# Optimization experiments

Measured on AMD Instinct MI355X. Metric: run time of the kernel, lower is better.

The kernel has to match this reference:

```python
import jax, jax.numpy as jnp
import numpy as np

H, W = 512, 512
N = H * W
NCLS = 4
D_BI, D_SP = 5, 2
THETA_ALPHA, THETA_BETA, THETA_GAMMA = 80.0, 0.0625, 3.0
BI_COMPAT, SP_COMPAT, COMPATIBILITY = 10.0, 3.0, -1.0
NUM_ITER = 10


def _build_lattice(feats):
    """Permutohedral lattice precompute (numpy, integer index construction).
    feats: [N, d]. Returns os [N,d+1] int32 (1-based), ws [N,d+1] float32,
    bn [d+1, M, 2] int32 (0 = missing neighbor), M."""
    feats = np.asarray(feats, np.float64)
    n, d = feats.shape
    inv_std = np.sqrt(2.0 / 3.0) * (d + 1)
    scale = inv_std / np.sqrt((np.arange(d) + 1.0) * (np.arange(d) + 2.0))
    cf = feats * scale
    # embedding matrix E: elevated = cf @ E.T lies on the hyperplane sum=0
    E = np.zeros((d + 1, d))
    E[0, :] = 1.0
    for j in range(1, d + 1):
        E[j, j:] = 1.0
        E[j, j - 1] = -j
    elevated = cf @ E.T  # [n, d+1]
    greedy = (np.rint(elevated / (d + 1)) * (d + 1)).astype(np.int64)
    diff = elevated - greedy
    idx = np.arange(d + 1)
    upper = idx[None, :] > idx[:, None]
    lower = idx[None, :] < idx[:, None]
    di = diff[:, :, None]
    dj = diff[:, None, :]
    rank = (((dj > di) & upper) | ((dj >= di) & lower)).sum(-1)
    rank = rank + greedy.sum(1, keepdims=True) // (d + 1)
    low = rank < 0
    rank = rank + np.where(low, d + 1, 0)
    greedy = greedy + np.where(low, d + 1, 0)
    high = rank > d
    rank = rank - np.where(high, d + 1, 0)
    greedy = greedy - np.where(high, d + 1, 0)
    # barycentric weights
    bary = np.zeros((n, d + 2))
    v = (elevated - greedy) / (d + 1)
    rows = np.repeat(np.arange(n), d + 1)
    np.add.at(bary, (rows, (d - rank).ravel()), v.ravel())
    np.add.at(bary, (rows, (d + 1 - rank).ravel()), -v.ravel())
    bary[:, 0] += 1.0 + bary[:, d + 1]
    ws = bary[:, : d + 1].astype(np.float32)
    # simplex vertex keys (first d coords; last is implied by zero-sum)
    keys = np.empty((n, d + 1, d), np.int64)
    for r in range(d + 1):
        keys[:, r, :] = (greedy + r - (d + 1) * (rank > d - r))[:, :d]
    flat = keys.reshape(-1, d)
    lo = flat.min(0) - (d + 1)
    hi = flat.max(0) + (d + 1)
    strides = np.cumprod(np.concatenate([[1], (hi - lo + 1)[:-1]]))
    coords = (flat - lo) @ strides
    uniq, first, inv = np.unique(coords, return_index=True, return_inverse=True)
    M = int(len(uniq))
    os_ = (inv.reshape(n, d + 1) + 1).astype(np.int32)
    ukeys = flat[first]
    bn = np.zeros((d + 1, M, 2), np.int32)
    for j in range(d + 1):
        n1 = ukeys - 1
        n2 = ukeys + 1
        if j < d:
            n1[:, j] = ukeys[:, j] + d
            n2[:, j] = ukeys[:, j] - d
        for t, nk in enumerate((n1, n2)):
            c = (nk - lo) @ strides
            pos = np.clip(np.searchsorted(uniq, c), 0, M - 1)
            bn[j, :, t] = np.where(uniq[pos] == c, pos + 1, 0)
    return os_, ws, bn, M


def setup_inputs() -> dict:
    key = jax.random.key(0)
    k1, k2 = jax.random.split(key)
    image = jax.random.uniform(k1, (H, W, 7), dtype=jnp.float32)
    unary = jax.random.normal(k2, (H, W, NCLS), dtype=jnp.float32)
    img = np.asarray(image)
    yy, xx = np.mgrid[0:H, 0:W].astype(np.float64)
    bifeat = np.concatenate(
        [(xx / THETA_ALPHA)[..., None], (yy / THETA_ALPHA)[..., None],
         img[..., :3] / THETA_BETA], axis=-1).reshape(N, D_BI)
    spfeat = np.stack([xx / THETA_GAMMA, yy / THETA_GAMMA], -1).reshape(N, D_SP)
    os_b, ws_b, bn_b, M_b = _build_lattice(bifeat)
    os_s, ws_s, bn_s, M_s = _build_lattice(spfeat)
    return {
        "unary": unary,
        "ws_bilateral": jnp.asarray(ws_b), "os_bilateral": jnp.asarray(os_b),
        "blur_neighbors_bilateral": jnp.asarray(bn_b), "M_bilateral": M_b,
        "ws_spatial": jnp.asarray(ws_s), "os_spatial": jnp.asarray(os_s),
        "blur_neighbors_spatial": jnp.asarray(bn_s), "M_spatial": M_s,
    }


def _perm_filter(values, os_, ws, bn, M, alpha):
    # values: [N, C]; splat -> blur -> slice
    d1 = os_.shape[1]
    C = values.shape[1]
    table = jnp.zeros((M + 1, C), values.dtype)  # row 0 = dummy (missing)
    table = table.at[os_.reshape(-1)].add(
        (values[:, None, :] * ws[:, :, None]).reshape(-1, C))
    for j in range(d1):  # [0.5, 1, 0.5] blur along each lattice axis
        table = table.at[1:].add(0.5 * (table[bn[j, :, 0]] + table[bn[j, :, 1]]))
    return alpha * jnp.einsum("nrc,nr->nc", table[os_], ws)


def _mean_field(unary, ws_b, os_b, bn_b, M_b, ws_s, os_s, bn_s, M_s):
    C = unary.shape[-1]
    u = unary.reshape(N, C)
    alpha_b = 1.0 / (1.0 + 2.0 ** (-D_BI))
    alpha_s = 1.0 / (1.0 + 2.0 ** (-D_SP))
    ones = jnp.ones((N, 1), u.dtype)
    inv_nb = 1.0 / (_perm_filter(ones, os_b, ws_b, bn_b, M_b, alpha_b) + 1e-20)
    inv_ns = 1.0 / (_perm_filter(ones, os_s, ws_s, bn_s, M_s, alpha_s) + 1e-20)
    Q = jax.nn.softmax(-u, axis=-1)
    for _ in range(NUM_ITER):
        msg = (BI_COMPAT * _perm_filter(Q, os_b, ws_b, bn_b, M_b, alpha_b) * inv_nb
               + SP_COMPAT * _perm_filter(Q, os_s, ws_s, bn_s, M_s, alpha_s) * inv_ns)
        Q = jax.nn.softmax(-u - COMPATIBILITY * msg, axis=-1)
    return Q.reshape(H, W, C)


def reference(unary, ws_bilateral, os_bilateral, blur_neighbors_bilateral, M_bilateral,
              ws_spatial, os_spatial, blur_neighbors_spatial, M_spatial):
    # Returns the refined marginals Q [H, W, NCLS]; the module's MAP output is
    # jnp.argmax(Q, -1) (kept soft here so fwd/bwd share one output).
    return _mean_field(unary, ws_bilateral, os_bilateral, blur_neighbors_bilateral,
                       M_bilateral, ws_spatial, os_spatial, blur_neighbors_spatial,
                       M_spatial)
```

## Files before the change

kernel.cpp:

```cpp
#include <hip/hip_runtime.h>

#define NPIX (512 * 512)
#define BLK 256

#define SCAN_T 256
#define SCAN_E 8
#define SCAN_CHUNK (SCAN_T * SCAN_E)

typedef _Float16 h4 __attribute__((ext_vector_type(4)));

constexpr float ALPHA_B = 32.0f / 33.0f;
constexpr float ALPHA_S = 0.8f;
constexpr float BI_COMPAT = 10.0f;
constexpr float SP_COMPAT = 3.0f;

__device__ __forceinline__ unsigned pack_ent(int n, float w) {
    float wc = fminf(fmaxf(w, 0.f), 1.f);
    unsigned iw = (unsigned)(wc * 16383.f + 0.5f);
    return (iw << 18) | (unsigned)n;
}
__device__ __forceinline__ int ent_pix(unsigned e) { return (int)(e & 0x3FFFFu); }
__device__ __forceinline__ float ent_w(unsigned e) {
    return (float)(e >> 18) * (1.0f / 16383.0f);
}

__device__ __forceinline__ float4 f4zero() { return make_float4(0.f, 0.f, 0.f, 0.f); }
__device__ __forceinline__ h4 h4zero() {
    h4 z; z.x = (_Float16)0.f; z.y = (_Float16)0.f; z.z = (_Float16)0.f; z.w = (_Float16)0.f;
    return z;
}

__global__ void k_softmax_init(const float4* __restrict__ u, float4* __restrict__ Q) {
    int n = blockIdx.x * BLK + threadIdx.x;
    if (n >= NPIX) return;
    float4 uu = u[n];
    float l0 = -uu.x, l1 = -uu.y, l2 = -uu.z, l3 = -uu.w;
    float m = fmaxf(fmaxf(l0, l1), fmaxf(l2, l3));
    float e0 = expf(l0 - m), e1 = expf(l1 - m), e2 = expf(l2 - m), e3 = expf(l3 - m);
    float inv = 1.0f / (e0 + e1 + e2 + e3);
    Q[n] = make_float4(e0 * inv, e1 * inv, e2 * inv, e3 * inv);
}

__global__ void k_count_softmax(const int* __restrict__ osb, const int* __restrict__ oss,
                                int* __restrict__ cntB, int* __restrict__ cntS,
                                const float4* __restrict__ u, float4* __restrict__ Q) {
    int n = blockIdx.x * BLK + threadIdx.x;
    if (n >= NPIX) return;
    float4 uu = u[n];
    float l0 = -uu.x, l1 = -uu.y, l2 = -uu.z, l3 = -uu.w;
    float m = fmaxf(fmaxf(l0, l1), fmaxf(l2, l3));
    float e0 = expf(l0 - m), e1 = expf(l1 - m), e2 = expf(l2 - m), e3 = expf(l3 - m);
    float inv = 1.0f / (e0 + e1 + e2 + e3);
    Q[n] = make_float4(e0 * inv, e1 * inv, e2 * inv, e3 * inv);
#pragma unroll
    for (int r = 0; r < 6; r++) atomicAdd(&cntB[osb[n * 6 + r]], 1);
#pragma unroll
    for (int r = 0; r < 3; r++) atomicAdd(&cntS[oss[n * 3 + r]], 1);
}

__global__ void k_chunk_sum(const int* __restrict__ counts, int V, int* __restrict__ csum) {
    __shared__ int lds[SCAN_T];
    int base = blockIdx.x * SCAN_CHUNK;
    int s = 0;
#pragma unroll
    for (int j = 0; j < SCAN_E; j++) {
        int idx = base + threadIdx.x * SCAN_E + j;
        if (idx < V) s += counts[idx];
    }
    lds[threadIdx.x] = s;
    __syncthreads();
    for (int off = SCAN_T / 2; off > 0; off >>= 1) {
        if ((int)threadIdx.x < off) lds[threadIdx.x] += lds[threadIdx.x + off];
        __syncthreads();
    }
    if (threadIdx.x == 0) csum[blockIdx.x] = lds[0];
}

__global__ void k_scan_csum(int* __restrict__ csum, int nchunks) {
    __shared__ int lds[SCAN_T];
    int carry = 0;
    for (int base = 0; base < nchunks; base += SCAN_T) {
        int idx = base + threadIdx.x;
        int v = (idx < nchunks) ? csum[idx] : 0;
        lds[threadIdx.x] = v;
        __syncthreads();
        for (int off = 1; off < SCAN_T; off <<= 1) {
            int t = ((int)threadIdx.x >= off) ? lds[threadIdx.x - off] : 0;
            __syncthreads();
            lds[threadIdx.x] += t;
            __syncthreads();
        }
        int incl = lds[threadIdx.x];
        int tile_total = lds[SCAN_T - 1];
        if (idx < nchunks) csum[idx] = incl - v + carry;
        carry += tile_total;
        __syncthreads();
    }
}

__global__ void k_chunk_scan(const int* __restrict__ counts, int V,
                             const int* __restrict__ csum, int* __restrict__ start,
                             int* __restrict__ cursor) {
    __shared__ int lds[SCAN_T];
    int base = blockIdx.x * SCAN_CHUNK;
    int local[SCAN_E];
    int s = 0;
#pragma unroll
    for (int j = 0; j < SCAN_E; j++) {
        int idx = base + threadIdx.x * SCAN_E + j;
        int c = (idx < V) ? counts[idx] : 0;
        local[j] = c;
        s += c;
    }
    lds[threadIdx.x] = s;
    __syncthreads();
    for (int off = 1; off < SCAN_T; off <<= 1) {
        int t = ((int)threadIdx.x >= off) ? lds[threadIdx.x - off] : 0;
        __syncthreads();
        lds[threadIdx.x] += t;
        __syncthreads();
    }
    int excl = lds[threadIdx.x] - s + csum[blockIdx.x];
#pragma unroll
    for (int j = 0; j < SCAN_E; j++) {
        int idx = base + threadIdx.x * SCAN_E + j;
        if (idx < V) { start[idx] = excl; cursor[idx] = excl; }
        excl += local[j];
    }
}

__global__ void k_fill_both(const int* __restrict__ osb, const float* __restrict__ wsb,
                            int* __restrict__ curB, unsigned* __restrict__ entB,
                            const int* __restrict__ oss, const float* __restrict__ wss,
                            int* __restrict__ curS, unsigned* __restrict__ entS) {
    int n = blockIdx.x * BLK + threadIdx.x;
    if (n >= NPIX) return;
#pragma unroll
    for (int r = 0; r < 6; r++) {
        int o = osb[n * 6 + r];
        int pos = atomicAdd(&curB[o], 1);
        entB[pos] = pack_ent(n, wsb[n * 6 + r]);
    }
#pragma unroll
    for (int r = 0; r < 3; r++) {
        int o = oss[n * 3 + r];
        int pos = atomicAdd(&curS[o], 1);
        entS[pos] = pack_ent(n, wss[n * 3 + r]);
    }
}

__global__ void k_gather1_both(const unsigned* __restrict__ entB, const int* __restrict__ startB,
                               int totB, int Vb, float* __restrict__ nB,
                               const unsigned* __restrict__ entS, const int* __restrict__ startS,
                               int totS, int Vs, float* __restrict__ nS) {
    int i = blockIdx.x * BLK + threadIdx.x;
    const unsigned* ent; const int* st; int tot, V, idx; float* out;
    if (i < Vb) { ent = entB; st = startB; tot = totB; V = Vb; out = nB; idx = i; }
    else {
        idx = i - Vb;
        if (idx >= Vs) return;
        ent = entS; st = startS; tot = totS; V = Vs; out = nS;
    }
    int s = st[idx];
    int e = (idx + 1 < V) ? st[idx + 1] : tot;
    float acc = 0.f;
    for (int k = s; k < e; k++) acc += ent_w(ent[k]);
    out[idx] = acc;
}

__global__ void k_gather4h_both(const unsigned* __restrict__ entB, const int* __restrict__ startB,
                                int totB, int Vb, h4* __restrict__ tB,
                                const unsigned* __restrict__ entS, const int* __restrict__ startS,
                                int totS, int Vs, h4* __restrict__ tS,
                                const float4* __restrict__ Q) {
    int i = blockIdx.x * BLK + threadIdx.x;
    const unsigned* ent; const int* st; int tot, V, idx; h4* out;
    if (i < Vb) { ent = entB; st = startB; tot = totB; V = Vb; out = tB; idx = i; }
    else {
        idx = i - Vb;
        if (idx >= Vs) return;
        ent = entS; st = startS; tot = totS; V = Vs; out = tS;
    }
    int s = st[idx];
    int e = (idx + 1 < V) ? st[idx + 1] : tot;
    float ax = 0.f, ay = 0.f, az = 0.f, aw = 0.f;
    for (int k = s; k < e; k++) {
        unsigned en = ent[k];
        float w = ent_w(en);
        float4 q = Q[ent_pix(en)];
        ax += w * q.x; ay += w * q.y; az += w * q.z; aw += w * q.w;
    }
    h4 h;
    h.x = (_Float16)ax; h.y = (_Float16)ay; h.z = (_Float16)az; h.w = (_Float16)aw;
    out[idx] = h;
}

__global__ void k_blur1(const float* __restrict__ in, float* __restrict__ out,
                        const int* __restrict__ bn, int M) {
    int i = blockIdx.x * BLK + threadIdx.x;
    if (i > M) return;
    if (i == 0) { out[0] = 0.f; return; }
    int n1 = bn[(size_t)(i - 1) * 2 + 0];
    int n2 = bn[(size_t)(i - 1) * 2 + 1];
    out[i] = in[i] + 0.5f * (in[n1] + in[n2]);
}

__global__ void k_blur1_both(const float* __restrict__ inB, float* __restrict__ outB,
                             const int* __restrict__ bnB, int Mb,
                             const float* __restrict__ inS, float* __restrict__ outS,
                             const int* __restrict__ bnS, int Ms) {
    int i = blockIdx.x * BLK + threadIdx.x;
    const float* in; float* out; const int* bn; int M, idx;
    if (i <= Mb) { in = inB; out = outB; bn = bnB; M = Mb; idx = i; }
    else {
        idx = i - (Mb + 1);
        if (idx > Ms) return;
        in = inS; out = outS; bn = bnS; M = Ms;
    }
    if (idx == 0) { out[0] = 0.f; return; }
    int n1 = bn[(size_t)(idx - 1) * 2 + 0];
    int n2 = bn[(size_t)(idx - 1) * 2 + 1];
    out[idx] = in[idx] + 0.5f * (in[n1] + in[n2]);
}

__global__ void k_blur4h(const h4* __restrict__ in, h4* __restrict__ out,
                         const int* __restrict__ bn, int M) {
    int i = blockIdx.x * BLK + threadIdx.x;
    if (i > M) return;
    if (i == 0) { out[0] = h4zero(); return; }
    int n1 = bn[(size_t)(i - 1) * 2 + 0];
    int n2 = bn[(size_t)(i - 1) * 2 + 1];
    h4 a = in[i], b = in[n1], c = in[n2];
    h4 o;
    o.x = (_Float16)((float)a.x + 0.5f * ((float)b.x + (float)c.x));
    o.y = (_Float16)((float)a.y + 0.5f * ((float)b.y + (float)c.y));
    o.z = (_Float16)((float)a.z + 0.5f * ((float)b.z + (float)c.z));
    o.w = (_Float16)((float)a.w + 0.5f * ((float)b.w + (float)c.w));
    out[i] = o;
}

__global__ void k_blur4h_both(const h4* __restrict__ inB, h4* __restrict__ outB,
                              const int* __restrict__ bnB, int Mb,
                              const h4* __restrict__ inS, h4* __restrict__ outS,
                              const int* __restrict__ bnS, int Ms) {
    int i = blockIdx.x * BLK + threadIdx.x;
    const h4* in; h4* out; const int* bn; int M, idx;
    if (i <= Mb) { in = inB; out = outB; bn = bnB; M = Mb; idx = i; }
    else {
        idx = i - (Mb + 1);
        if (idx > Ms) return;
        in = inS; out = outS; bn = bnS; M = Ms;
    }
    if (idx == 0) { out[0] = h4zero(); return; }
    int n1 = bn[(size_t)(idx - 1) * 2 + 0];
    int n2 = bn[(size_t)(idx - 1) * 2 + 1];
    h4 a = in[idx], b = in[n1], c = in[n2];
    h4 o;
    o.x = (_Float16)((float)a.x + 0.5f * ((float)b.x + (float)c.x));
    o.y = (_Float16)((float)a.y + 0.5f * ((float)b.y + (float)c.y));
    o.z = (_Float16)((float)a.z + 0.5f * ((float)b.z + (float)c.z));
    o.w = (_Float16)((float)a.w + 0.5f * ((float)b.w + (float)c.w));
    out[idx] = o;
}

__global__ void k_norm_prescale(const float* __restrict__ nTb, const float* __restrict__ wsb,
                                const int* __restrict__ osb,
                                const float* __restrict__ nTs, const float* __restrict__ wss,
                                const int* __restrict__ oss,
                                float* __restrict__ wsbp, float* __restrict__ wssp) {
    int n = blockIdx.x * BLK + threadIdx.x;
    if (n >= NPIX) return;
    float sb = 0.f;
#pragma unroll
    for (int r = 0; r < 6; r++) sb += wsb[n * 6 + r] * nTb[osb[n * 6 + r]];
    float cb = BI_COMPAT * ALPHA_B / (ALPHA_B * sb + 1e-20f);
#pragma unroll
    for (int r = 0; r < 6; r++) wsbp[n * 6 + r] = wsb[n * 6 + r] * cb;
    float ss = 0.f;
#pragma unroll
    for (int r = 0; r < 3; r++) ss += wss[n * 3 + r] * nTs[oss[n * 3 + r]];
    float cs = SP_COMPAT * ALPHA_S / (ALPHA_S * ss + 1e-20f);
#pragma unroll
    for (int r = 0; r < 3; r++) wssp[n * 3 + r] = wss[n * 3 + r] * cs;
}

__global__ void k_slice_combine_h(const float4* __restrict__ u,
                                  const h4* __restrict__ tb, const float* __restrict__ wsbp,
                                  const int* __restrict__ osb,
                                  const h4* __restrict__ ts, const float* __restrict__ wssp,
                                  const int* __restrict__ oss,
                                  float4* __restrict__ Qout) {
    int n = blockIdx.x * BLK + threadIdx.x;
    if (n >= NPIX) return;
    float4 uu = u[n];
    float l0 = -uu.x, l1 = -uu.y, l2 = -uu.z, l3 = -uu.w;
#pragma unroll
    for (int r = 0; r < 6; r++) {
        float w = wsbp[n * 6 + r];
        h4 t = tb[osb[n * 6 + r]];
        l0 += w * (float)t.x; l1 += w * (float)t.y; l2 += w * (float)t.z; l3 += w * (float)t.w;
    }
#pragma unroll
    for (int r = 0; r < 3; r++) {
        float w = wssp[n * 3 + r];
        h4 t = ts[oss[n * 3 + r]];
        l0 += w * (float)t.x; l1 += w * (float)t.y; l2 += w * (float)t.z; l3 += w * (float)t.w;
    }
    float m = fmaxf(fmaxf(l0, l1), fmaxf(l2, l3));
    float e0 = expf(l0 - m), e1 = expf(l1 - m), e2 = expf(l2 - m), e3 = expf(l3 - m);
    float inv = 1.0f / (e0 + e1 + e2 + e3);
    Qout[n] = make_float4(e0 * inv, e1 * inv, e2 * inv, e3 * inv);
}

template <int D1>
__global__ void k_splat1(const float* __restrict__ ws, const int* __restrict__ os,
                         float* __restrict__ table) {
    int n = blockIdx.x * BLK + threadIdx.x;
    if (n >= NPIX) return;
#pragma unroll
    for (int r = 0; r < D1; r++) atomicAdd(&table[os[n * D1 + r]], ws[n * D1 + r]);
}

template <int D1>
__global__ void k_splat4(const float4* __restrict__ Q, const float* __restrict__ ws,
                         const int* __restrict__ os, float* __restrict__ table) {
    int n = blockIdx.x * BLK + threadIdx.x;
    if (n >= NPIX) return;
    float4 q = Q[n];
#pragma unroll
    for (int r = 0; r < D1; r++) {
        float w = ws[n * D1 + r];
        int o = os[n * D1 + r];
        float* t = table + 4 * (size_t)o;
        atomicAdd(t + 0, q.x * w);
        atomicAdd(t + 1, q.y * w);
        atomicAdd(t + 2, q.z * w);
        atomicAdd(t + 3, q.w * w);
    }
}

__global__ void k_blur4(const float4* __restrict__ in, float4* __restrict__ out,
                        const int* __restrict__ bn, int M) {
    int i = blockIdx.x * BLK + threadIdx.x;
    if (i > M) return;
    if (i == 0) { out[0] = f4zero(); return; }
    int n1 = bn[(size_t)(i - 1) * 2 + 0];
    int n2 = bn[(size_t)(i - 1) * 2 + 1];
    float4 a = in[i], b = in[n1], c = in[n2];
    out[i] = make_float4(a.x + 0.5f * (b.x + c.x), a.y + 0.5f * (b.y + c.y),
                         a.z + 0.5f * (b.z + c.z), a.w + 0.5f * (b.w + c.w));
}

template <int D1>
__global__ void k_norm_slice(const float* __restrict__ table, const float* __restrict__ ws,
                             const int* __restrict__ os, float alpha,
                             float* __restrict__ inv_out) {
    int n = blockIdx.x * BLK + threadIdx.x;
    if (n >= NPIX) return;
    float s = 0.f;
#pragma unroll
    for (int r = 0; r < D1; r++) s += ws[n * D1 + r] * table[os[n * D1 + r]];
    inv_out[n] = 1.0f / (alpha * s + 1e-20f);
}

__global__ void k_slice_combine(const float4* __restrict__ u,
                                const float4* __restrict__ tb, const float* __restrict__ wsb,
                                const int* __restrict__ osb,
                                const float4* __restrict__ ts, const float* __restrict__ wss,
                                const int* __restrict__ oss,
                                const float* __restrict__ inv_nb,
                                const float* __restrict__ inv_ns,
                                float4* __restrict__ Qout) {
    int n = blockIdx.x * BLK + threadIdx.x;
    if (n >= NPIX) return;
    float4 ab = f4zero();
#pragma unroll
    for (int r = 0; r < 6; r++) {
        float w = wsb[n * 6 + r];
        float4 t = tb[osb[n * 6 + r]];
        ab.x += w * t.x; ab.y += w * t.y; ab.z += w * t.z; ab.w += w * t.w;
    }
    float4 as = f4zero();
#pragma unroll
    for (int r = 0; r < 3; r++) {
        float w = wss[n * 3 + r];
        float4 t = ts[oss[n * 3 + r]];
        as.x += w * t.x; as.y += w * t.y; as.z += w * t.z; as.w += w * t.w;
    }
    float cb = BI_COMPAT * ALPHA_B * inv_nb[n];
    float cs = SP_COMPAT * ALPHA_S * inv_ns[n];
    float4 uu = u[n];
    float l0 = -uu.x + cb * ab.x + cs * as.x;
    float l1 = -uu.y + cb * ab.y + cs * as.y;
    float l2 = -uu.z + cb * ab.z + cs * as.z;
    float l3 = -uu.w + cb * ab.w + cs * as.w;
    float m = fmaxf(fmaxf(l0, l1), fmaxf(l2, l3));
    float e0 = expf(l0 - m), e1 = expf(l1 - m), e2 = expf(l2 - m), e3 = expf(l3 - m);
    float inv = 1.0f / (e0 + e1 + e2 + e3);
    Qout[n] = make_float4(e0 * inv, e1 * inv, e2 * inv, e3 * inv);
}

extern "C" void kernel_launch(void* const* d_in, const int* in_sizes, int n_in,
                              void* d_out, int out_size, void* d_ws, size_t ws_size,
                              hipStream_t stream) {
    const float* unary = (const float*)d_in[0];
    const float* wsb   = (const float*)d_in[1];
    const int*   osb   = (const int*)d_in[2];
    const int*   bnb   = (const int*)d_in[3];
    const float* wss   = (const float*)d_in[5];
    const int*   oss   = (const int*)d_in[6];
    const int*   bns   = (const int*)d_in[7];
    const int Mb = in_sizes[3] / 12;
    const int Ms = in_sizes[7] / 6;
    const int Vb = Mb + 1, Vs = Ms + 1;
    const int totB = NPIX * 6, totS = NPIX * 3;

    float* Q = (float*)d_out;

    char* p = (char*)d_ws;
    auto alloc = [&](size_t nbytes) -> void* {
        void* r = (void*)p;
        p += (nbytes + 15) & ~(size_t)15;
        return r;
    };
    h4*   tAb  = (h4*)alloc((size_t)Vb * 8);
    h4*   tBb  = (h4*)alloc((size_t)Vb * 8);
    h4*   tAs  = (h4*)alloc((size_t)Vs * 8);
    h4*   tBs  = (h4*)alloc((size_t)Vs * 8);
    float* nAb = (float*)alloc((size_t)Vb * 4);
    float* nBb = (float*)alloc((size_t)Vb * 4);
    float* nAs = (float*)alloc((size_t)Vs * 4);
    float* nBs = (float*)alloc((size_t)Vs * 4);
    float* wsbp = (float*)alloc((size_t)NPIX * 6 * 4);
    float* wssp = (float*)alloc((size_t)NPIX * 3 * 4);
    int*  startB  = (int*)alloc((size_t)Vb * 4);
    int*  cursorB = (int*)alloc((size_t)Vb * 4);
    unsigned* entB = (unsigned*)alloc((size_t)totB * 4);
    int*  startS  = (int*)alloc((size_t)Vs * 4);
    int*  cursorS = (int*)alloc((size_t)Vs * 4);
    unsigned* entS = (unsigned*)alloc((size_t)totS * 4);
    int*  csum    = (int*)alloc(8192 * 4);
    size_t need = (size_t)(p - (char*)d_ws);
    bool use_gather = need <= ws_size;

    dim3 blk(BLK);
    dim3 gN((NPIX + BLK - 1) / BLK);
    dim3 gVb((Vb + BLK - 1) / BLK);
    dim3 gVBS((Vb + Vs + BLK - 1) / BLK);

    if (use_gather) {
        int nchB = (Vb + SCAN_CHUNK - 1) / SCAN_CHUNK;
        int nchS = (Vs + SCAN_CHUNK - 1) / SCAN_CHUNK;
        hipMemsetAsync(cursorB, 0, (size_t)Vb * 4, stream);
        hipMemsetAsync(cursorS, 0, (size_t)Vs * 4, stream);
        k_count_softmax<<<gN, blk, 0, stream>>>(osb, oss, cursorB, cursorS,
                                                (const float4*)unary, (float4*)Q);
        k_chunk_sum<<<dim3(nchB), dim3(SCAN_T), 0, stream>>>(cursorB, Vb, csum);
        k_scan_csum<<<dim3(1), dim3(SCAN_T), 0, stream>>>(csum, nchB);
        k_chunk_scan<<<dim3(nchB), dim3(SCAN_T), 0, stream>>>(cursorB, Vb, csum, startB, cursorB);
        k_chunk_sum<<<dim3(nchS), dim3(SCAN_T), 0, stream>>>(cursorS, Vs, csum);
        k_scan_csum<<<dim3(1), dim3(SCAN_T), 0, stream>>>(csum, nchS);
        k_chunk_scan<<<dim3(nchS), dim3(SCAN_T), 0, stream>>>(cursorS, Vs, csum, startS, cursorS);
        k_fill_both<<<gN, blk, 0, stream>>>(osb, wsb, cursorB, entB, oss, wss, cursorS, entS);

        k_gather1_both<<<gVBS, blk, 0, stream>>>(entB, startB, totB, Vb, nAb,
                                                 entS, startS, totS, Vs, nAs);
        {
            float* a = nAb; float* b = nBb;
            float* as_ = nAs; float* bs_ = nBs;
            for (int j = 0; j < 3; j++) {
                k_blur1_both<<<gVBS, blk, 0, stream>>>(a, b, bnb + (size_t)j * Mb * 2, Mb,
                                                       as_, bs_, bns + (size_t)j * Ms * 2, Ms);
                float* t = a; a = b; b = t;
                t = as_; as_ = bs_; bs_ = t;
            }
            for (int j = 3; j < 6; j++) {
                k_blur1<<<gVb, blk, 0, stream>>>(a, b, bnb + (size_t)j * Mb * 2, Mb);
                float* t = a; a = b; b = t;
            }
            k_norm_prescale<<<gN, blk, 0, stream>>>(a, wsb, osb, as_, wss, oss, wsbp, wssp);
        }

        for (int it = 0; it < 10; it++) {
            k_gather4h_both<<<gVBS, blk, 0, stream>>>(entB, startB, totB, Vb, tAb,
                                                      entS, startS, totS, Vs, tAs,
                                                      (const float4*)Q);
            h4* a = tAb; h4* b = tBb;
            h4* as_ = tAs; h4* bs_ = tBs;
            for (int j = 0; j < 3; j++) {
                k_blur4h_both<<<gVBS, blk, 0, stream>>>(a, b, bnb + (size_t)j * Mb * 2, Mb,
                                                        as_, bs_, bns + (size_t)j * Ms * 2, Ms);
                h4* t = a; a = b; b = t;
                t = as_; as_ = bs_; bs_ = t;
            }
            for (int j = 3; j < 6; j++) {
                k_blur4h<<<gVb, blk, 0, stream>>>(a, b, bnb + (size_t)j * Mb * 2, Mb);
                h4* t = a; a = b; b = t;
            }
            k_slice_combine_h<<<gN, blk, 0, stream>>>((const float4*)unary,
                                                      a, wsbp, osb, as_, wssp, oss,
                                                      (float4*)Q);
        }
    } else {
        char* q = (char*)d_ws;
        auto alloc2 = [&](size_t nbytes) -> void* {
            void* r = (void*)q;
            q += (nbytes + 15) & ~(size_t)15;
            return r;
        };
        float* fAb = (float*)alloc2((size_t)Vb * 4 * sizeof(float));
        float* fBb = (float*)alloc2((size_t)Vb * 4 * sizeof(float));
        float* fAs = (float*)alloc2((size_t)Vs * 4 * sizeof(float));
        float* fBs = (float*)alloc2((size_t)Vs * 4 * sizeof(float));
        float* inv_nb = (float*)alloc2(NPIX * sizeof(float));
        float* inv_ns = (float*)alloc2(NPIX * sizeof(float));
        dim3 gMb((Mb + 1 + BLK - 1) / BLK);
        dim3 gMs((Ms + 1 + BLK - 1) / BLK);

        hipMemsetAsync(fAb, 0, (size_t)Vb * sizeof(float), stream);
        k_splat1<6><<<gN, blk, 0, stream>>>(wsb, osb, fAb);
        {
            float* a = fAb; float* b = fBb;
            for (int j = 0; j < 6; j++) {
                k_blur1<<<gMb, blk, 0, stream>>>(a, b, bnb + (size_t)j * Mb * 2, Mb);
                float* t = a; a = b; b = t;
            }
            k_norm_slice<6><<<gN, blk, 0, stream>>>(a, wsb, osb, ALPHA_B, inv_nb);
        }
        hipMemsetAsync(fAs, 0, (size_t)Vs * sizeof(float), stream);
        k_splat1<3><<<gN, blk, 0, stream>>>(wss, oss, fAs);
        {
            float* a = fAs; float* b = fBs;
            for (int j = 0; j < 3; j++) {
                k_blur1<<<gMs, blk, 0, stream>>>(a, b, bns + (size_t)j * Ms * 2, Ms);
                float* t = a; a = b; b = t;
            }
            k_norm_slice<3><<<gN, blk, 0, stream>>>(a, wss, oss, ALPHA_S, inv_ns);
        }
        k_softmax_init<<<gN, blk, 0, stream>>>((const float4*)unary, (float4*)Q);
        for (int it = 0; it < 10; it++) {
            hipMemsetAsync(fAb, 0, (size_t)Vb * 4 * sizeof(float), stream);
            k_splat4<6><<<gN, blk, 0, stream>>>((const float4*)Q, wsb, osb, fAb);
            float* a = fAb; float* b = fBb;
            for (int j = 0; j < 6; j++) {
                k_blur4<<<gMb, blk, 0, stream>>>((const float4*)a, (float4*)b,
                                                 bnb + (size_t)j * Mb * 2, Mb);
                float* t = a; a = b; b = t;
            }
            float* finb = a;
            hipMemsetAsync(fAs, 0, (size_t)Vs * 4 * sizeof(float), stream);
            k_splat4<3><<<gN, blk, 0, stream>>>((const float4*)Q, wss, oss, fAs);
            float* as_ = fAs; float* bs_ = fBs;
            for (int j = 0; j < 3; j++) {
                k_blur4<<<gMs, blk, 0, stream>>>((const float4*)as_, (float4*)bs_,
                                                 bns + (size_t)j * Ms * 2, Ms);
                float* t = as_; as_ = bs_; bs_ = t;
            }
            float* fins = as_;
            k_slice_combine<<<gN, blk, 0, stream>>>((const float4*)unary,
                                                    (const float4*)finb, wsb, osb,
                                                    (const float4*)fins, wss, oss,
                                                    inv_nb, inv_ns, (float4*)Q);
        }
    }
}
```

Measured before the change: 1.011 ms.

## Build vertex entry lists via atomic linked lists and merged scan

Replaces the count-then-atomic-cursor fill with a single pass that counts and links entries into per-vertex linked lists, then a compact kernel walks each list into a contiguous CSR array. Bilateral and spatial vertices share one combined start/entry array and a single scan. This aims to cut a full atomic pass and several scan launches from setup. In exchange, each thread walks its list serially with dependent loads, and the next array is aliased onto the prescaled-weight buffer.

```diff
diff --git a/kernel.cpp b/kernel.cpp
--- a/kernel.cpp
+++ b/kernel.cpp
@@ -6,6 +6,10 @@
 #define SCAN_T 256
 #define SCAN_E 8
 #define SCAN_CHUNK (SCAN_T * SCAN_E)
+
+#define TOTB (NPIX * 6)
+#define TOTS (NPIX * 3)
+#define TOTE (NPIX * 9)
 
 typedef _Float16 h4 __attribute__((ext_vector_type(4)));
 
@@ -41,9 +45,11 @@
     Q[n] = make_float4(e0 * inv, e1 * inv, e2 * inv, e3 * inv);
 }
 
-__global__ void k_count_softmax(const int* __restrict__ osb, const int* __restrict__ oss,
-                                int* __restrict__ cntB, int* __restrict__ cntS,
-                                const float4* __restrict__ u, float4* __restrict__ Q) {
+__global__ void k_count_link_softmax(const int* __restrict__ osb, const int* __restrict__ oss,
+                                     int* __restrict__ cnt, int* __restrict__ head,
+                                     int* __restrict__ next,
+                                     const float4* __restrict__ u, float4* __restrict__ Q,
+                                     int Vb) {
     int n = blockIdx.x * BLK + threadIdx.x;
     if (n >= NPIX) return;
     float4 uu = u[n];
@@ -53,9 +59,19 @@
     float inv = 1.0f / (e0 + e1 + e2 + e3);
     Q[n] = make_float4(e0 * inv, e1 * inv, e2 * inv, e3 * inv);
 #pragma unroll
-    for (int r = 0; r < 6; r++) atomicAdd(&cntB[osb[n * 6 + r]], 1);
-#pragma unroll
-    for (int r = 0; r < 3; r++) atomicAdd(&cntS[oss[n * 3 + r]], 1);
+    for (int r = 0; r < 6; r++) {
+        int o = osb[n * 6 + r];
+        int e = n * 6 + r;
+        atomicAdd(&cnt[o], 1);
+        next[e] = atomicExch(&head[o], e);
+    }
+#pragma unroll
+    for (int r = 0; r < 3; r++) {
+        int o = Vb + oss[n * 3 + r];
+        int e = TOTB + n * 3 + r;
+        atomicAdd(&cnt[o], 1);
+        next[e] = atomicExch(&head[o], e);
+    }
 }
 
 __global__ void k_chunk_sum(const int* __restrict__ counts, int V, int* __restrict__ csum) {
@@ -99,8 +115,7 @@
 }
 
 __global__ void k_chunk_scan(const int* __restrict__ counts, int V,
-                             const int* __restrict__ csum, int* __restrict__ start,
-                             int* __restrict__ cursor) {
+                             const int* __restrict__ csum, int* __restrict__ start) {
     __shared__ int lds[SCAN_T];
     int base = blockIdx.x * SCAN_CHUNK;
     int local[SCAN_E];
@@ -124,65 +139,56 @@
 #pragma unroll
     for (int j = 0; j < SCAN_E; j++) {
         int idx = base + threadIdx.x * SCAN_E + j;
-        if (idx < V) { start[idx] = excl; cursor[idx] = excl; }
+        if (idx < V) start[idx] = excl;
         excl += local[j];
     }
 }
 
-__global__ void k_fill_both(const int* __restrict__ osb, const float* __restrict__ wsb,
-                            int* __restrict__ curB, unsigned* __restrict__ entB,
-                            const int* __restrict__ oss, const float* __restrict__ wss,
-                            int* __restrict__ curS, unsigned* __restrict__ entS) {
-    int n = blockIdx.x * BLK + threadIdx.x;
-    if (n >= NPIX) return;
-#pragma unroll
-    for (int r = 0; r < 6; r++) {
-        int o = osb[n * 6 + r];
-        int pos = atomicAdd(&curB[o], 1);
-        entB[pos] = pack_ent(n, wsb[n * 6 + r]);
-    }
-#pragma unroll
-    for (int r = 0; r < 3; r++) {
-        int o = oss[n * 3 + r];
-        int pos = atomicAdd(&curS[o], 1);
-        entS[pos] = pack_ent(n, wss[n * 3 + r]);
-    }
-}
-
-__global__ void k_gather1_both(const unsigned* __restrict__ entB, const int* __restrict__ startB,
-                               int totB, int Vb, float* __restrict__ nB,
-                               const unsigned* __restrict__ entS, const int* __restrict__ startS,
-                               int totS, int Vs, float* __restrict__ nS) {
-    int i = blockIdx.x * BLK + threadIdx.x;
-    const unsigned* ent; const int* st; int tot, V, idx; float* out;
-    if (i < Vb) { ent = entB; st = startB; tot = totB; V = Vb; out = nB; idx = i; }
-    else {
-        idx = i - Vb;
-        if (idx >= Vs) return;
-        ent = entS; st = startS; tot = totS; V = Vs; out = nS;
-    }
-    int s = st[idx];
-    int e = (idx + 1 < V) ? st[idx + 1] : tot;
+__global__ void k_compact(const int* __restrict__ head, const int* __restrict__ next,
+                          const int* __restrict__ start,
+                          const float* __restrict__ wsb, const float* __restrict__ wss,
+                          unsigned* __restrict__ ent, int V, int Vb) {
+    int o = blockIdx.x * BLK + threadIdx.x;
+    if (o >= V) return;
+    int p = start[o];
+    int e = head[o];
+    if (o < Vb) {
+        while (e >= 0) {
+            unsigned n = (unsigned)e / 6u;
+            ent[p++] = pack_ent((int)n, wsb[e]);
+            e = next[e];
+        }
+    } else {
+        while (e >= 0) {
+            int ee = e - TOTB;
+            unsigned n = (unsigned)ee / 3u;
+            ent[p++] = pack_ent((int)n, wss[ee]);
+            e = next[e];
+        }
+    }
+}
+
+__global__ void k_gather1_both(const unsigned* __restrict__ ent, const int* __restrict__ start,
+                               int V, int Vb,
+                               float* __restrict__ nB, float* __restrict__ nS) {
+    int i = blockIdx.x * BLK + threadIdx.x;
+    if (i >= V) return;
+    int s = start[i];
+    int e = (i + 1 < V) ? start[i + 1] : TOTE;
     float acc = 0.f;
     for (int k = s; k < e; k++) acc += ent_w(ent[k]);
-    out[idx] = acc;
-}
-
-__global__ void k_gather4h_both(const unsigned* __restrict__ entB, const int* __restrict__ startB,
-                                int totB, int Vb, h4* __restrict__ tB,
-                                const unsigned* __restrict__ entS, const int* __restrict__ startS,
-                                int totS, int Vs, h4* __restrict__ tS,
+    if (i < Vb) nB[i] = acc;
+    else nS[i - Vb] = acc;
+}
+
+__global__ void k_gather4h_both(const unsigned* __restrict__ ent, const int* __restrict__ start,
+                                int V, int Vb,
+                                h4* __restrict__ tB, h4* __restrict__ tS,
                                 const float4* __restrict__ Q) {
     int i = blockIdx.x * BLK + threadIdx.x;
-    const unsigned* ent; const int* st; int tot, V, idx; h4* out;
-    if (i < Vb) { ent = entB; st = startB; tot = totB; V = Vb; out = tB; idx = i; }
-    else {
-        idx = i - Vb;
-        if (idx >= Vs) return;
-        ent = entS; st = startS; tot = totS; V = Vs; out = tS;
-    }
-    int s = st[idx];
-    int e = (idx + 1 < V) ? st[idx + 1] : tot;
+    if (i >= V) return;
+    int s = start[i];
+    int e = (i + 1 < V) ? start[i + 1] : TOTE;
     float ax = 0.f, ay = 0.f, az = 0.f, aw = 0.f;
     for (int k = s; k < e; k++) {
         unsigned en = ent[k];
@@ -192,7 +198,8 @@
     }
     h4 h;
     h.x = (_Float16)ax; h.y = (_Float16)ay; h.z = (_Float16)az; h.w = (_Float16)aw;
-    out[idx] = h;
+    if (i < Vb) tB[i] = h;
+    else tS[i - Vb] = h;
 }
 
 __global__ void k_blur1(const float* __restrict__ in, float* __restrict__ out,
@@ -413,7 +420,7 @@
     const int Mb = in_sizes[3] / 12;
     const int Ms = in_sizes[7] / 6;
     const int Vb = Mb + 1, Vs = Ms + 1;
-    const int totB = NPIX * 6, totS = NPIX * 3;
+    const int V = Vb + Vs;
 
     float* Q = (float*)d_out;
 
@@ -433,44 +440,38 @@
     float* nBs = (float*)alloc((size_t)Vs * 4);
     float* wsbp = (float*)alloc((size_t)NPIX * 6 * 4);
     float* wssp = (float*)alloc((size_t)NPIX * 3 * 4);
-    int*  startB  = (int*)alloc((size_t)Vb * 4);
-    int*  cursorB = (int*)alloc((size_t)Vb * 4);
-    unsigned* entB = (unsigned*)alloc((size_t)totB * 4);
-    int*  startS  = (int*)alloc((size_t)Vs * 4);
-    int*  cursorS = (int*)alloc((size_t)Vs * 4);
-    unsigned* entS = (unsigned*)alloc((size_t)totS * 4);
-    int*  csum    = (int*)alloc(8192 * 4);
+    int*   next = (int*)wsbp;
+    int*  start = (int*)alloc((size_t)V * 4);
+    int*  cnt   = (int*)alloc((size_t)V * 4);
+    int*  head  = (int*)alloc((size_t)V * 4);
+    unsigned* ent = (unsigned*)alloc((size_t)TOTE * 4);
+    int*  csum  = (int*)alloc(8192 * 4);
     size_t need = (size_t)(p - (char*)d_ws);
     bool use_gather = need <= ws_size;
 
     dim3 blk(BLK);
     dim3 gN((NPIX + BLK - 1) / BLK);
     dim3 gVb((Vb + BLK - 1) / BLK);
-    dim3 gVBS((Vb + Vs + BLK - 1) / BLK);
+    dim3 gV((V + BLK - 1) / BLK);
 
     if (use_gather) {
-        int nchB = (Vb + SCAN_CHUNK - 1) / SCAN_CHUNK;
-        int nchS = (Vs + SCAN_CHUNK - 1) / SCAN_CHUNK;
-        hipMemsetAsync(cursorB, 0, (size_t)Vb * 4, stream);
-        hipMemsetAsync(cursorS, 0, (size_t)Vs * 4, stream);
-        k_count_softmax<<<gN, blk, 0, stream>>>(osb, oss, cursorB, cursorS,
-                                                (const float4*)unary, (float4*)Q);
-        k_chunk_sum<<<dim3(nchB), dim3(SCAN_T), 0, stream>>>(cursorB, Vb, csum);
-        k_scan_csum<<<dim3(1), dim3(SCAN_T), 0, stream>>>(csum, nchB);
-        k_chunk_scan<<<dim3(nchB), dim3(SCAN_T), 0, stream>>>(cursorB, Vb, csum, startB, cursorB);
-        k_chunk_sum<<<dim3(nchS), dim3(SCAN_T), 0, stream>>>(cursorS, Vs, csum);
-        k_scan_csum<<<dim3(1), dim3(SCAN_T), 0, stream>>>(csum, nchS);
-        k_chunk_scan<<<dim3(nchS), dim3(SCAN_T), 0, stream>>>(cursorS, Vs, csum, startS, cursorS);
-        k_fill_both<<<gN, blk, 0, stream>>>(osb, wsb, cursorB, entB, oss, wss, cursorS, entS);
-
-        k_gather1_both<<<gVBS, blk, 0, stream>>>(entB, startB, totB, Vb, nAb,
-                                                 entS, startS, totS, Vs, nAs);
+        int nch = (V + SCAN_CHUNK - 1) / SCAN_CHUNK;
+        hipMemsetAsync(cnt, 0, (size_t)V * 4, stream);
+        hipMemsetAsync(head, 0xFF, (size_t)V * 4, stream);
+        k_count_link_softmax<<<gN, blk, 0, stream>>>(osb, oss, cnt, head, next,
+                                                     (const float4*)unary, (float4*)Q, Vb);
+        k_chunk_sum<<<dim3(nch), dim3(SCAN_T), 0, stream>>>(cnt, V, csum);
+        k_scan_csum<<<dim3(1), dim3(SCAN_T), 0, stream>>>(csum, nch);
+        k_chunk_scan<<<dim3(nch), dim3(SCAN_T), 0, stream>>>(cnt, V, csum, start);
+        k_compact<<<gV, blk, 0, stream>>>(head, next, start, wsb, wss, ent, V, Vb);
+
+        k_gather1_both<<<gV, blk, 0, stream>>>(ent, start, V, Vb, nAb, nAs);
         {
             float* a = nAb; float* b = nBb;
             float* as_ = nAs; float* bs_ = nBs;
             for (int j = 0; j < 3; j++) {
-                k_blur1_both<<<gVBS, blk, 0, stream>>>(a, b, bnb + (size_t)j * Mb * 2, Mb,
-                                                       as_, bs_, bns + (size_t)j * Ms * 2, Ms);
+                k_blur1_both<<<gV, blk, 0, stream>>>(a, b, bnb + (size_t)j * Mb * 2, Mb,
+                                                     as_, bs_, bns + (size_t)j * Ms * 2, Ms);
                 float* t = a; a = b; b = t;
                 t = as_; as_ = bs_; bs_ = t;
             }
@@ -482,14 +483,13 @@
         }
 
         for (int it = 0; it < 10; it++) {
-            k_gather4h_both<<<gVBS, blk, 0, stream>>>(entB, startB, totB, Vb, tAb,
-                                                      entS, startS, totS, Vs, tAs,
-                                                      (const float4*)Q);
+            k_gather4h_both<<<gV, blk, 0, stream>>>(ent, start, V, Vb, tAb, tAs,
+                                                    (const float4*)Q);
             h4* a = tAb; h4* b = tBb;
             h4* as_ = tAs; h4* bs_ = tBs;
             for (int j = 0; j < 3; j++) {
-                k_blur4h_both<<<gVBS, blk, 0, stream>>>(a, b, bnb + (size_t)j * Mb * 2, Mb,
-                                                        as_, bs_, bns + (size_t)j * Ms * 2, Ms);
+                k_blur4h_both<<<gV, blk, 0, stream>>>(a, b, bnb + (size_t)j * Mb * 2, Mb,
+                                                      as_, bs_, bns + (size_t)j * Ms * 2, Ms);
                 h4* t = a; a = b; b = t;
                 t = as_; as_ = bs_; bs_ = t;
             }
```

Measured after the change: 1.075 ms. +6.3%, slower.
